# Kernel optimization log

Hardware: AMD Instinct MI355X
Metric: run time of the kernel (lower is better)

Reference implementation:

```python
import jax, jax.numpy as jnp
import numpy as np

N_NODES = 50000
N_EDGES = 800000
IN_DIM = 64
HEADS = 8
OUT_DIM = 8
CLAMP = 5.0
EPS = 1e-8


def _xavier(key, shape, fan_in, fan_out):
    std = float(np.sqrt(2.0 / (fan_in + fan_out)))
    return jax.random.normal(key, shape, jnp.float32) * std


def setup_inputs() -> dict:
    key = jax.random.key(0)
    ks = jax.random.split(key, 16)
    HD = HEADS * OUT_DIM
    return {
        "x": jax.random.normal(ks[0], (N_NODES, IN_DIM), jnp.float32),
        "edge_attr": jax.random.normal(ks[1], (N_EDGES, IN_DIM), jnp.float32),
        "edge_index": jax.random.randint(ks[2], (2, N_EDGES), 0, N_NODES, jnp.int64),
        "Wq": _xavier(ks[3], (IN_DIM, HD), IN_DIM, HD),
        "bq": jnp.zeros((HD,), jnp.float32),
        "Wk": _xavier(ks[4], (IN_DIM, HD), IN_DIM, HD),
        "bk": jnp.zeros((HD,), jnp.float32),
        "We": _xavier(ks[5], (IN_DIM, 2 * HD), IN_DIM, 2 * HD),
        "be": jnp.zeros((2 * HD,), jnp.float32),
        "Wv": _xavier(ks[6], (IN_DIM, HD), IN_DIM, HD),
        "bv": jnp.zeros((HD,), jnp.float32),
        "Aw": _xavier(ks[7], (OUT_DIM, HEADS, 1), OUT_DIM * HEADS, 1),
        "VeRow": _xavier(ks[8], (OUT_DIM, HEADS, OUT_DIM), OUT_DIM * HEADS, OUT_DIM),
    }


def _segment_softmax(score, seg, num_segments):
    # score: [E, H, 1], seg: [E] destination node ids
    m = jax.ops.segment_max(score, seg, num_segments=num_segments)
    m = jnp.where(jnp.isfinite(m), m, 0.0)  # empty segments -> -inf guard
    e = jnp.exp(score - m[seg])
    s = jax.ops.segment_sum(e, seg, num_segments=num_segments)
    return e / (s[seg] + 1e-16)


def reference(x, edge_attr, edge_index, Wq, bq, Wk, bk, We, be, Wv, bv, Aw, VeRow):
    n = x.shape[0]
    Q_h = (x @ Wq + bq).reshape(n, HEADS, OUT_DIM)
    K_h = (x @ Wk + bk).reshape(n, HEADS, OUT_DIM)
    V_h = (x @ Wv + bv).reshape(n, HEADS, OUT_DIM)
    E_proj = (edge_attr @ We + be).reshape(-1, HEADS, 2 * OUT_DIM)
    E_w, E_b = E_proj[:, :, :OUT_DIM], E_proj[:, :, OUT_DIM:]

    src, dst = edge_index[0], edge_index[1]
    score = K_h[src] + Q_h[dst]                       # [E, H, D]
    score = score * E_w
    # signed-sqrt
    score = jnp.sqrt(jax.nn.relu(score) + EPS) - jnp.sqrt(jax.nn.relu(-score) + EPS)
    score = score + E_b
    e_t = score                                       # act = Identity
    wE = score.reshape(score.shape[0], -1)            # [E, H*D]

    s = jnp.einsum('ehd,dhc->ehc', score, Aw)         # [E, H, 1]
    s = jnp.clip(s, -CLAMP, CLAMP)
    attn = _segment_softmax(s, dst, n)                # [E, H, 1]

    msg = V_h[src] * attn                             # [E, H, D]
    wV = jax.ops.segment_sum(msg, dst, num_segments=n)
    rowV = jax.ops.segment_sum(e_t * attn, dst, num_segments=n)
    wV = wV + jnp.einsum('nhd,dhc->nhc', rowV, VeRow)
    return wV, wE
```

## Files before the change

kernel.cpp:

```cpp
#include <hip/hip_runtime.h>
#include <math.h>

#define N_NODES 50000
#define N_EDGES 800000
#define CLAMP_V 5.0f
#define EPS_V   1e-8f

__global__ __launch_bounds__(192) void qkv_kernel(
    const float* __restrict__ x,
    const float* __restrict__ Wq, const float* __restrict__ bq,
    const float* __restrict__ Wk, const float* __restrict__ bk,
    const float* __restrict__ Wv, const float* __restrict__ bv,
    float* __restrict__ qkv)
{
  __shared__ float sW[64][192];
  __shared__ float sb[192];
  __shared__ float sa[16][68];
  const int t = threadIdx.x;
  for (int k = 0; k < 64; k++) {
    float w;
    if (t < 64)       w = Wq[k*64 + t];
    else if (t < 128) w = Wk[k*64 + (t-64)];
    else              w = Wv[k*64 + (t-128)];
    sW[k][t] = w;
  }
  sb[t] = (t < 64) ? bq[t] : (t < 128) ? bk[t-64] : bv[t-128];
  const int n0 = blockIdx.x * 16;
  for (int idx = t; idx < 256; idx += 192) {
    int node = idx >> 4, kq = idx & 15;
    *(float4*)&sa[node][kq*4] = *(const float4*)&x[(size_t)(n0+node)*64 + kq*4];
  }
  __syncthreads();
  float acc[16];
  #pragma unroll
  for (int j = 0; j < 16; j++) acc[j] = 0.f;
  for (int k4 = 0; k4 < 16; k4++) {
    float wq[4];
    #pragma unroll
    for (int q = 0; q < 4; q++) wq[q] = sW[k4*4+q][t];
    #pragma unroll
    for (int jh = 0; jh < 2; jh++) {
      float4 av[8];
      #pragma unroll
      for (int jj = 0; jj < 8; jj++) av[jj] = *(const float4*)&sa[jh*8+jj][k4*4];
      #pragma unroll
      for (int jj = 0; jj < 8; jj++) {
        acc[jh*8+jj] += av[jj].x*wq[0] + av[jj].y*wq[1] + av[jj].z*wq[2] + av[jj].w*wq[3];
      }
    }
  }
  const float b = sb[t];
  #pragma unroll
  for (int j = 0; j < 16; j++) qkv[(size_t)(n0+j)*192 + t] = acc[j] + b;
}

__global__ __launch_bounds__(256) void edge_kernel(
    const float* __restrict__ edge_attr,
    const int*   __restrict__ eidx,
    const float* __restrict__ We, const float* __restrict__ be,
    const float* __restrict__ Aw,
    const float* __restrict__ qkv,
    float* __restrict__ wE, float* __restrict__ sExp)
{
  __shared__ float sW[64][136];
  __shared__ float sbe[128];
  __shared__ float sAw[64];
  __shared__ float sA[128][68];
  const int t = threadIdx.x;
  for (int i = t; i < 2048; i += 256) {
    int k = i >> 5, c = (i & 31) * 4;
    *(float4*)&sW[k][c + 8*(c>>6)] = *(const float4*)&We[(size_t)k*128 + c];
  }
  if (t < 128)       sbe[t] = be[t];
  else if (t < 192)  sAw[t-128] = Aw[t-128];
  const int e0 = blockIdx.x * 128;
  for (int i = t; i < 2048; i += 256) {
    int e = i >> 4, kq = i & 15;
    *(float4*)&sA[e][(kq ^ ((e>>3)&3)) * 4] =
        *(const float4*)&edge_attr[(size_t)(e0+e)*64 + kq*4];
  }
  __syncthreads();
  const int te = t >> 4;
  const int g = t & 15, h = g >> 1, dq = g & 1;
  const int cw = h*16 + dq*4, cb = cw + 8;
  const int cwp = cw + 8*(h>>2), cbp = cb + 8*(h>>2);
  const int swa = te & 3;
  float4 accw[8], accb[8];
  #pragma unroll
  for (int j = 0; j < 8; j++) { accw[j] = make_float4(0,0,0,0); accb[j] = make_float4(0,0,0,0); }
  for (int kq = 0; kq < 16; kq++) {
    float4 av[8];
    const int kcol = (kq ^ swa) * 4;
    #pragma unroll
    for (int j = 0; j < 8; j++) av[j] = *(const float4*)&sA[te*8+j][kcol];
    #pragma unroll
    for (int q = 0; q < 4; q++) {
      const int k = kq*4 + q;
      const float4 ww = *(const float4*)&sW[k][cwp];
      const float4 wb = *(const float4*)&sW[k][cbp];
      #pragma unroll
      for (int j = 0; j < 8; j++) {
        const float a = (q==0) ? av[j].x : (q==1) ? av[j].y : (q==2) ? av[j].z : av[j].w;
        accw[j].x += a*ww.x; accw[j].y += a*ww.y; accw[j].z += a*ww.z; accw[j].w += a*ww.w;
        accb[j].x += a*wb.x; accb[j].y += a*wb.y; accb[j].z += a*wb.z; accb[j].w += a*wb.w;
      }
    }
  }
  const float4 bw = *(const float4*)&sbe[cw];
  const float4 bb = *(const float4*)&sbe[cb];
  const int d0 = dq * 4;
  const float awc0 = sAw[(d0+0)*8+h], awc1 = sAw[(d0+1)*8+h];
  const float awc2 = sAw[(d0+2)*8+h], awc3 = sAw[(d0+3)*8+h];
  #pragma unroll
  for (int j = 0; j < 8; j++) {
    const int e   = e0 + te*8 + j;
    const int src = eidx[e];
    const int dst = eidx[N_EDGES + e];
    const float4 kv = *(const float4*)&qkv[(size_t)src*192 + 64 + h*8 + d0];
    const float4 qv = *(const float4*)&qkv[(size_t)dst*192 +      h*8 + d0];
    const float s0 = (kv.x+qv.x)*(accw[j].x+bw.x);
    const float s1 = (kv.y+qv.y)*(accw[j].y+bw.y);
    const float s2 = (kv.z+qv.z)*(accw[j].z+bw.z);
    const float s3 = (kv.w+qv.w)*(accw[j].w+bw.w);
    const float r0 = sqrtf(fmaxf(s0,0.f)+EPS_V) - sqrtf(fmaxf(-s0,0.f)+EPS_V) + (accb[j].x+bb.x);
    const float r1 = sqrtf(fmaxf(s1,0.f)+EPS_V) - sqrtf(fmaxf(-s1,0.f)+EPS_V) + (accb[j].y+bb.y);
    const float r2 = sqrtf(fmaxf(s2,0.f)+EPS_V) - sqrtf(fmaxf(-s2,0.f)+EPS_V) + (accb[j].z+bb.z);
    const float r3 = sqrtf(fmaxf(s3,0.f)+EPS_V) - sqrtf(fmaxf(-s3,0.f)+EPS_V) + (accb[j].w+bb.w);
    *(float4*)&wE[(size_t)e*64 + h*8 + d0] = make_float4(r0,r1,r2,r3);
    float ps = r0*awc0 + r1*awc1 + r2*awc2 + r3*awc3;
    ps += __shfl_xor(ps, 1, 64);
    if (dq == 0) {
      const float sc = fminf(fmaxf(ps, -CLAMP_V), CLAMP_V);
      sExp[(size_t)e*8 + h] = expf(sc);
    }
  }
}

__global__ __launch_bounds__(256) void count_kernel(const int* __restrict__ eidx,
                                                    int* __restrict__ deg)
{
  const int e = blockIdx.x*256 + threadIdx.x;
  if (e < N_EDGES) atomicAdd(&deg[eidx[N_EDGES + e]], 1);
}

__global__ __launch_bounds__(1024) void scan_kernel(const int* __restrict__ deg,
                                                    int* __restrict__ row_start,
                                                    int* __restrict__ cursor)
{
  __shared__ int buf[1024];
  __shared__ int carry;
  const int t = threadIdx.x;
  if (t == 0) carry = 0;
  __syncthreads();
  for (int base = 0; base < N_NODES; base += 1024) {
    const int i = base + t;
    const int v = (i < N_NODES) ? deg[i] : 0;
    buf[t] = v;
    __syncthreads();
    int sum = v;
    for (int off = 1; off < 1024; off <<= 1) {
      const int other = (t >= off) ? buf[t-off] : 0;
      __syncthreads();
      sum += other;
      buf[t] = sum;
      __syncthreads();
    }
    const int base_c = carry;
    const int excl = base_c + sum - v;
    if (i < N_NODES) { row_start[i] = excl; cursor[i] = excl; }
    __syncthreads();
    if (t == 1023) carry = base_c + sum;
    __syncthreads();
  }
  if (t == 0) row_start[N_NODES] = carry;
}

__global__ __launch_bounds__(256) void scatter_kernel(const int* __restrict__ eidx,
                                                      int* __restrict__ cursor,
                                                      int* __restrict__ edge_ord)
{
  const int e = blockIdx.x*256 + threadIdx.x;
  if (e < N_EDGES) {
    const int pos = atomicAdd(&cursor[eidx[N_EDGES + e]], 1);
    edge_ord[pos] = e;
  }
}

__global__ __launch_bounds__(256) void node_kernel(
    const int*   __restrict__ eidx,
    const int*   __restrict__ row_start,
    const int*   __restrict__ edge_ord,
    const float* __restrict__ sExp,
    const float* __restrict__ qkv,
    const float* __restrict__ wE,
    const float* __restrict__ VeRow,
    float* __restrict__ wV)
{
  __shared__ float sVe[512];
  const int t = threadIdx.x;
  for (int i = t; i < 512; i += 256) sVe[i] = VeRow[i];
  __syncthreads();
  const int lane = t & 63;
  const int node = blockIdx.x*4 + (t >> 6);
  const int h = lane >> 3;
  const int rs = row_start[node], re = row_start[node+1];
  float denom = 0.f;
  for (int j = rs; j < re; j++)
    denom += sExp[(size_t)edge_ord[j]*8 + h];
  const float rden = 1.0f / (denom + 1e-16f);
  float accW = 0.f, accR = 0.f;
  for (int j = rs; j < re; j++) {
    const int eid = edge_ord[j];
    const float attn = sExp[(size_t)eid*8 + h] * rden;
    const int src = eidx[eid];
    accW += qkv[(size_t)src*192 + 128 + lane] * attn;
    accR += wE[(size_t)eid*64 + lane] * attn;
  }
  float val = accW;
  #pragma unroll
  for (int dd = 0; dd < 8; dd++) {
    const float rv = __shfl(accR, h*8 + dd, 64);
    val += rv * sVe[dd*64 + lane];
  }
  wV[(size_t)node*64 + lane] = val;
}

extern "C" void kernel_launch(void* const* d_in, const int* in_sizes, int n_in,
                              void* d_out, int out_size, void* d_ws, size_t ws_size,
                              hipStream_t stream)
{
  const float* x         = (const float*)d_in[0];
  const float* edge_attr = (const float*)d_in[1];
  const int*   eidx      = (const int*)  d_in[2];
  const float* Wq        = (const float*)d_in[3];
  const float* bq        = (const float*)d_in[4];
  const float* Wk        = (const float*)d_in[5];
  const float* bk        = (const float*)d_in[6];
  const float* We        = (const float*)d_in[7];
  const float* be        = (const float*)d_in[8];
  const float* Wv        = (const float*)d_in[9];
  const float* bv        = (const float*)d_in[10];
  const float* Aw        = (const float*)d_in[11];
  const float* VeRow     = (const float*)d_in[12];

  float* out = (float*)d_out;
  float* wV  = out;
  float* wE  = out + (size_t)N_NODES * 64;

  char* ws = (char*)d_ws;
  float* qkv      = (float*)(ws);
  float* sExp     = (float*)(ws + 38400000);
  int*   deg      = (int*)  (ws + 64000000);
  int*   row_start= (int*)  (ws + 64200000);
  int*   cursor   = (int*)  (ws + 64400016);
  int*   edge_ord = (int*)  (ws + 64600016);

  hipMemsetAsync(deg, 0, N_NODES * sizeof(int), stream);
  qkv_kernel   <<<3125,  192, 0, stream>>>(x, Wq, bq, Wk, bk, Wv, bv, qkv);
  edge_kernel  <<<6250,  256, 0, stream>>>(edge_attr, eidx, We, be, Aw, qkv, wE, sExp);
  count_kernel <<<3125,  256, 0, stream>>>(eidx, deg);
  scan_kernel  <<<1,    1024, 0, stream>>>(deg, row_start, cursor);
  scatter_kernel<<<3125, 256, 0, stream>>>(eidx, cursor, edge_ord);
  node_kernel  <<<12500, 256, 0, stream>>>(eidx, row_start, edge_ord, sExp, qkv, wE, VeRow, wV);
}
```

Before: 1.029 ms.

## Split edge GEMM K-loop, serial-chunk scan, permuted src, single-pass node softmax

Edge kernel now stages We and edge_attr in two K-halves, which cuts its shared memory and so may allow more resident blocks, at the cost of an extra barrier. The scan kernel has each thread sum a 49-element chunk before one block-wide scan, replacing 49 serial block scans. The scatter kernel also writes src indices in destination order, so the node kernel skips the eidx indirection. The node kernel folds the softmax denominator into a single unrolled-by-4 pass with nontemporal wE loads and normalises once at the end, removing the second pass over sExp.

```diff
diff --git a/kernel.cpp b/kernel.cpp
--- a/kernel.cpp
+++ b/kernel.cpp
@@ -62,24 +62,12 @@
     const float* __restrict__ qkv,
     float* __restrict__ wE, float* __restrict__ sExp)
 {
-  __shared__ float sW[64][136];
+  __shared__ float sW[32][136];
+  __shared__ float sA[128][32];
   __shared__ float sbe[128];
   __shared__ float sAw[64];
-  __shared__ float sA[128][68];
-  const int t = threadIdx.x;
-  for (int i = t; i < 2048; i += 256) {
-    int k = i >> 5, c = (i & 31) * 4;
-    *(float4*)&sW[k][c + 8*(c>>6)] = *(const float4*)&We[(size_t)k*128 + c];
-  }
-  if (t < 128)       sbe[t] = be[t];
-  else if (t < 192)  sAw[t-128] = Aw[t-128];
+  const int t = threadIdx.x;
   const int e0 = blockIdx.x * 128;
-  for (int i = t; i < 2048; i += 256) {
-    int e = i >> 4, kq = i & 15;
-    *(float4*)&sA[e][(kq ^ ((e>>3)&3)) * 4] =
-        *(const float4*)&edge_attr[(size_t)(e0+e)*64 + kq*4];
-  }
-  __syncthreads();
   const int te = t >> 4;
   const int g = t & 15, h = g >> 1, dq = g & 1;
   const int cw = h*16 + dq*4, cb = cw + 8;
@@ -88,24 +76,41 @@
   float4 accw[8], accb[8];
   #pragma unroll
   for (int j = 0; j < 8; j++) { accw[j] = make_float4(0,0,0,0); accb[j] = make_float4(0,0,0,0); }
-  for (int kq = 0; kq < 16; kq++) {
-    float4 av[8];
-    const int kcol = (kq ^ swa) * 4;
-    #pragma unroll
-    for (int j = 0; j < 8; j++) av[j] = *(const float4*)&sA[te*8+j][kcol];
-    #pragma unroll
-    for (int q = 0; q < 4; q++) {
-      const int k = kq*4 + q;
-      const float4 ww = *(const float4*)&sW[k][cwp];
-      const float4 wb = *(const float4*)&sW[k][cbp];
-      #pragma unroll
-      for (int j = 0; j < 8; j++) {
-        const float a = (q==0) ? av[j].x : (q==1) ? av[j].y : (q==2) ? av[j].z : av[j].w;
-        accw[j].x += a*ww.x; accw[j].y += a*ww.y; accw[j].z += a*ww.z; accw[j].w += a*ww.w;
-        accb[j].x += a*wb.x; accb[j].y += a*wb.y; accb[j].z += a*wb.z; accb[j].w += a*wb.w;
+  if (t < 128)       sbe[t] = be[t];
+  else if (t < 192)  sAw[t-128] = Aw[t-128];
+
+  for (int ph = 0; ph < 2; ph++) {
+    if (ph) __syncthreads();
+    for (int i = t; i < 1024; i += 256) {
+      int k = i >> 5, c = (i & 31) * 4;
+      *(float4*)&sW[k][c + 8*(c>>6)] = *(const float4*)&We[(size_t)(ph*32+k)*128 + c];
+    }
+    for (int i = t; i < 1024; i += 256) {
+      int e = i >> 3, kq = i & 7;
+      *(float4*)&sA[e][(kq ^ ((e>>3)&3)) * 4] =
+          *(const float4*)&edge_attr[(size_t)(e0+e)*64 + ph*32 + kq*4];
+    }
+    __syncthreads();
+    for (int kq = 0; kq < 8; kq++) {
+      float4 av[8];
+      const int kcol = (kq ^ swa) * 4;
+      #pragma unroll
+      for (int j = 0; j < 8; j++) av[j] = *(const float4*)&sA[te*8+j][kcol];
+      #pragma unroll
+      for (int q = 0; q < 4; q++) {
+        const int k = kq*4 + q;
+        const float4 ww = *(const float4*)&sW[k][cwp];
+        const float4 wb = *(const float4*)&sW[k][cbp];
+        #pragma unroll
+        for (int j = 0; j < 8; j++) {
+          const float a = (q==0) ? av[j].x : (q==1) ? av[j].y : (q==2) ? av[j].z : av[j].w;
+          accw[j].x += a*ww.x; accw[j].y += a*ww.y; accw[j].z += a*ww.z; accw[j].w += a*ww.w;
+          accb[j].x += a*wb.x; accb[j].y += a*wb.y; accb[j].z += a*wb.z; accb[j].w += a*wb.w;
+        }
       }
     }
   }
+
   const float4 bw = *(const float4*)&sbe[cw];
   const float4 bb = *(const float4*)&sbe[cb];
   const int d0 = dq * 4;
@@ -148,48 +153,44 @@
                                                     int* __restrict__ cursor)
 {
   __shared__ int buf[1024];
-  __shared__ int carry;
-  const int t = threadIdx.x;
-  if (t == 0) carry = 0;
+  const int t = threadIdx.x;
+  const int beg = t * 49;
+  const int end = (beg + 49 < N_NODES) ? beg + 49 : N_NODES;
+  int sum = 0;
+  for (int i = beg; i < end; i++) sum += deg[i];
+  buf[t] = sum;
   __syncthreads();
-  for (int base = 0; base < N_NODES; base += 1024) {
-    const int i = base + t;
-    const int v = (i < N_NODES) ? deg[i] : 0;
-    buf[t] = v;
+  for (int off = 1; off < 1024; off <<= 1) {
+    const int v = (t >= off) ? buf[t-off] : 0;
     __syncthreads();
-    int sum = v;
-    for (int off = 1; off < 1024; off <<= 1) {
-      const int other = (t >= off) ? buf[t-off] : 0;
-      __syncthreads();
-      sum += other;
-      buf[t] = sum;
-      __syncthreads();
-    }
-    const int base_c = carry;
-    const int excl = base_c + sum - v;
-    if (i < N_NODES) { row_start[i] = excl; cursor[i] = excl; }
+    buf[t] += v;
     __syncthreads();
-    if (t == 1023) carry = base_c + sum;
-    __syncthreads();
-  }
-  if (t == 0) row_start[N_NODES] = carry;
+  }
+  int run = (t == 0) ? 0 : buf[t-1];
+  for (int i = beg; i < end; i++) {
+    const int d = deg[i];
+    row_start[i] = run; cursor[i] = run; run += d;
+  }
+  if (t == 1023) row_start[N_NODES] = buf[1023];
 }
 
 __global__ __launch_bounds__(256) void scatter_kernel(const int* __restrict__ eidx,
                                                       int* __restrict__ cursor,
-                                                      int* __restrict__ edge_ord)
+                                                      int* __restrict__ edge_ord,
+                                                      int* __restrict__ src_perm)
 {
   const int e = blockIdx.x*256 + threadIdx.x;
   if (e < N_EDGES) {
     const int pos = atomicAdd(&cursor[eidx[N_EDGES + e]], 1);
     edge_ord[pos] = e;
+    src_perm[pos] = eidx[e];
   }
 }
 
 __global__ __launch_bounds__(256) void node_kernel(
-    const int*   __restrict__ eidx,
     const int*   __restrict__ row_start,
     const int*   __restrict__ edge_ord,
+    const int*   __restrict__ src_perm,
     const float* __restrict__ sExp,
     const float* __restrict__ qkv,
     const float* __restrict__ wE,
@@ -204,25 +205,42 @@
   const int node = blockIdx.x*4 + (t >> 6);
   const int h = lane >> 3;
   const int rs = row_start[node], re = row_start[node+1];
-  float denom = 0.f;
-  for (int j = rs; j < re; j++)
-    denom += sExp[(size_t)edge_ord[j]*8 + h];
-  const float rden = 1.0f / (denom + 1e-16f);
-  float accW = 0.f, accR = 0.f;
-  for (int j = rs; j < re; j++) {
+  float accU = 0.f, accR = 0.f, accD = 0.f;
+  int j = rs;
+  for (; j + 4 <= re; j += 4) {
+    const int e0 = edge_ord[j],   e1 = edge_ord[j+1];
+    const int e2 = edge_ord[j+2], e3 = edge_ord[j+3];
+    const int s0 = src_perm[j],   s1 = src_perm[j+1];
+    const int s2 = src_perm[j+2], s3 = src_perm[j+3];
+    const float w0 = sExp[(size_t)e0*8 + h], w1 = sExp[(size_t)e1*8 + h];
+    const float w2 = sExp[(size_t)e2*8 + h], w3 = sExp[(size_t)e3*8 + h];
+    const float t0 = __builtin_nontemporal_load(&wE[(size_t)e0*64 + lane]);
+    const float t1 = __builtin_nontemporal_load(&wE[(size_t)e1*64 + lane]);
+    const float t2 = __builtin_nontemporal_load(&wE[(size_t)e2*64 + lane]);
+    const float t3 = __builtin_nontemporal_load(&wE[(size_t)e3*64 + lane]);
+    const float v0 = qkv[(size_t)s0*192 + 128 + lane];
+    const float v1 = qkv[(size_t)s1*192 + 128 + lane];
+    const float v2 = qkv[(size_t)s2*192 + 128 + lane];
+    const float v3 = qkv[(size_t)s3*192 + 128 + lane];
+    accD += (w0 + w1) + (w2 + w3);
+    accU += w0*v0; accU += w1*v1; accU += w2*v2; accU += w3*v3;
+    accR += w0*t0; accR += w1*t1; accR += w2*t2; accR += w3*t3;
+  }
+  for (; j < re; j++) {
     const int eid = edge_ord[j];
-    const float attn = sExp[(size_t)eid*8 + h] * rden;
-    const int src = eidx[eid];
-    accW += qkv[(size_t)src*192 + 128 + lane] * attn;
-    accR += wE[(size_t)eid*64 + lane] * attn;
-  }
-  float val = accW;
+    const int src = src_perm[j];
+    const float w = sExp[(size_t)eid*8 + h];
+    accD += w;
+    accU += w * qkv[(size_t)src*192 + 128 + lane];
+    accR += w * __builtin_nontemporal_load(&wE[(size_t)eid*64 + lane]);
+  }
+  float val = accU;
   #pragma unroll
   for (int dd = 0; dd < 8; dd++) {
     const float rv = __shfl(accR, h*8 + dd, 64);
     val += rv * sVe[dd*64 + lane];
   }
-  wV[(size_t)node*64 + lane] = val;
+  wV[(size_t)node*64 + lane] = val * (1.0f / (accD + 1e-16f));
 }
 
 extern "C" void kernel_launch(void* const* d_in, const int* in_sizes, int n_in,
@@ -252,14 +270,15 @@
   float* sExp     = (float*)(ws + 38400000);
   int*   deg      = (int*)  (ws + 64000000);
   int*   row_start= (int*)  (ws + 64200000);
-  int*   cursor   = (int*)  (ws + 64400016);
-  int*   edge_ord = (int*)  (ws + 64600016);
+  int*   cursor   = (int*)  (ws + 64400208);
+  int*   edge_ord = (int*)  (ws + 64600208);
+  int*   src_perm = (int*)  (ws + 67800208);
 
   hipMemsetAsync(deg, 0, N_NODES * sizeof(int), stream);
-  qkv_kernel   <<<3125,  192, 0, stream>>>(x, Wq, bq, Wk, bk, Wv, bv, qkv);
-  edge_kernel  <<<6250,  256, 0, stream>>>(edge_attr, eidx, We, be, Aw, qkv, wE, sExp);
-  count_kernel <<<3125,  256, 0, stream>>>(eidx, deg);
-  scan_kernel  <<<1,    1024, 0, stream>>>(deg, row_start, cursor);
-  scatter_kernel<<<3125, 256, 0, stream>>>(eidx, cursor, edge_ord);
-  node_kernel  <<<12500, 256, 0, stream>>>(eidx, row_start, edge_ord, sExp, qkv, wE, VeRow, wV);
-}
+  qkv_kernel    <<<3125,  192, 0, stream>>>(x, Wq, bq, Wk, bk, Wv, bv, qkv);
+  edge_kernel   <<<6250,  256, 0, stream>>>(edge_attr, eidx, We, be, Aw, qkv, wE, sExp);
+  count_kernel  <<<3125,  256, 0, stream>>>(eidx, deg);
+  scan_kernel   <<<1,    1024, 0, stream>>>(deg, row_start, cursor);
+  scatter_kernel<<<3125,  256, 0, stream>>>(eidx, cursor, edge_ord, src_perm);
+  node_kernel   <<<12500, 256, 0, stream>>>(row_start, edge_ord, src_perm, sExp, qkv, wE, VeRow, wV);
+}
```

Result: faster. 866.8 us (-15.7%).
